# Kernel optimization log

Measured on AMD Instinct MI355X. Metric: run time of the kernel, lower is better.

Reference implementation:

```python
import jax, jax.numpy as jnp
import numpy as np

N_NODES = 50000
N_EDGES = 1_600_000
IN_DIM = 256
HIDDEN = 256
OUT_DIM = 48
K = 10
ALPHA = 0.5


def _ppr_temp(K, alpha):
    # PPR init from GPR_prop: temp[k] = alpha*(1-alpha)^k, temp[K] = (1-alpha)^K
    t = alpha * (1 - alpha) ** np.arange(K + 1, dtype=np.float32)
    t[-1] = (1 - alpha) ** K
    return jnp.asarray(t, dtype=jnp.float32)


def setup_inputs() -> dict:
    key = jax.random.key(0)
    ks = jax.random.split(key, 7)
    x = jax.random.normal(ks[0], (N_NODES, IN_DIM), dtype=jnp.float32)
    edge_index = jax.random.randint(ks[1], (2, N_EDGES), 0, N_NODES, dtype=jnp.int64)
    # Linear layers (torch Linear: y = x @ W.T + b); store as [in, out]
    lim1 = 1.0 / np.sqrt(IN_DIM)
    W1 = jax.random.uniform(ks[2], (IN_DIM, HIDDEN), jnp.float32, -lim1, lim1)
    b1 = jax.random.uniform(ks[3], (HIDDEN,), jnp.float32, -lim1, lim1)
    lim2 = 1.0 / np.sqrt(HIDDEN)
    W2 = jax.random.uniform(ks[4], (HIDDEN, OUT_DIM), jnp.float32, -lim2, lim2)
    b2 = jax.random.uniform(ks[5], (OUT_DIM,), jnp.float32, -lim2, lim2)
    temp = _ppr_temp(K, ALPHA)
    return {"x": x, "edge_index": edge_index, "W1": W1, "b1": b1,
            "W2": W2, "b2": b2, "temp": temp}


def reference(x, edge_index, W1, b1, W2, b2, temp):
    N = x.shape[0]
    # MLP head (dropout in eval mode -> identity)
    h = jax.nn.relu(x @ W1 + b1)
    h = h @ W2 + b2  # [N, OUT_DIM]

    # GCN normalization with self-loops: norm_e = deg^-1/2[src] * deg^-1/2[dst]
    loops = jnp.arange(N, dtype=edge_index.dtype)
    src = jnp.concatenate([edge_index[0], loops])
    dst = jnp.concatenate([edge_index[1], loops])
    deg = jnp.zeros((N,), dtype=h.dtype).at[dst].add(1.0)
    dinv = jax.lax.rsqrt(jnp.maximum(deg, 1e-12))
    norm = (dinv[src] * dinv[dst])[:, None]  # [E+N, 1]

    # K-hop propagation with learned gamma mixing
    def step(carry, gamma):
        hk, hidden = carry
        msg = norm * hk[src]                              # gather + scale
        hk = jax.ops.segment_sum(msg, dst, num_segments=N)  # scatter-add
        return (hk, hidden + gamma * hk), None

    (_, hidden), _ = jax.lax.scan(step, (h, temp[0] * h), temp[1:])
    return jax.nn.log_softmax(hidden, axis=1)
```

## Files before the change

kernel.cpp:

```cpp
#include <hip/hip_runtime.h>
#include <hip/hip_fp16.h>
#include <math.h>

#define BSH    9
#define BNODES 512
#define NBMAX  128
#define CAP2   24576
#define ECHUNK 6144

typedef short bf16x8 __attribute__((ext_vector_type(8)));
typedef float f32x4 __attribute__((ext_vector_type(4)));

__device__ __forceinline__ unsigned f2b(float f) {
    union { float f; unsigned u; } x; x.f = f;
    return (x.u + 0x7fffu + ((x.u >> 16) & 1u)) >> 16;
}


__global__ __launch_bounds__(256) void k_zero(int* __restrict__ p, int n) {
    int i = blockIdx.x * 256 + threadIdx.x;
    if (i < n) p[i] = 0;
}


__global__ __launch_bounds__(256) void k_castx(const float4* __restrict__ x, uint4* __restrict__ xb, int n8) {
    int i = blockIdx.x * 256 + threadIdx.x;
    if (i >= n8) return;
    float4 f0 = x[2 * i], f1 = x[2 * i + 1];
    uint4 o;
    o.x = f2b(f0.x) | (f2b(f0.y) << 16);
    o.y = f2b(f0.z) | (f2b(f0.w) << 16);
    o.z = f2b(f1.x) | (f2b(f1.y) << 16);
    o.w = f2b(f1.z) | (f2b(f1.w) << 16);
    xb[i] = o;
}

__global__ __launch_bounds__(256) void k_castw(const float* __restrict__ W1, const float* __restrict__ W2,
                                               unsigned short* __restrict__ w1t, unsigned short* __restrict__ w2t) {
    int i = blockIdx.x * 256 + threadIdx.x;
    if (i < 65536) {
        int n = i >> 8, k = i & 255;
        w1t[i] = (unsigned short)f2b(W1[k * 256 + n]);
    } else if (i < 65536 + 12288) {
        int j = i - 65536;
        int n = j >> 8, k = j & 255;
        w2t[j] = (unsigned short)f2b(W2[k * 48 + n]);
    }
}


__global__ __launch_bounds__(256) void k_bin(const int* __restrict__ src, const int* __restrict__ dst,
                                             int* __restrict__ bktcnt, unsigned* __restrict__ stage,
                                             int E, int NB) {
    __shared__ unsigned ecache[ECHUNK];
    __shared__ int lcnt[NBMAX], lbase[NBMAX], lcur[NBMAX];
    const int t = threadIdx.x;
    for (int i = t; i < NBMAX; i += 256) { lcnt[i] = 0; lcur[i] = 0; }
    const int e0 = blockIdx.x * ECHUNK;
    const int m = min(ECHUNK, E - e0);
    __syncthreads();
    for (int i = t; i < m; i += 256) {
        int s = src[e0 + i], d = dst[e0 + i];
        ecache[i] = ((unsigned)d << 16) | (unsigned)s;
        atomicAdd(&lcnt[d >> BSH], 1);
    }
    __syncthreads();
    if (t < NB) lbase[t] = lcnt[t] ? atomicAdd(&bktcnt[t], lcnt[t]) : 0;
    __syncthreads();
    for (int i = t; i < m; i += 256) {
        unsigned p = ecache[i];
        int b = (int)(p >> (16 + BSH));
        int pos = lbase[b] + atomicAdd(&lcur[b], 1);
        if (pos < CAP2) stage[(size_t)b * CAP2 + pos] = p;
    }
}


__global__ __launch_bounds__(512) void k_cnt(const unsigned* __restrict__ stage,
                                             const int* __restrict__ bktcnt,
                                             int* __restrict__ cnt,
                                             float* __restrict__ dinv, float* __restrict__ dinv2,
                                             float* __restrict__ sdeg, int N) {
    __shared__ int dcnt[BNODES];
    const int b = blockIdx.x, t = threadIdx.x;
    dcnt[t] = 0;
    __syncthreads();
    const int m = min(bktcnt[b], CAP2);
    const unsigned* st = stage + (size_t)b * CAP2;
    for (int i = t; i < m; i += 512)
        atomicAdd(&dcnt[(st[i] >> 16) & (BNODES - 1)], 1);
    __syncthreads();
    int node = b * BNODES + t;
    if (node <= N) {
        int c = dcnt[t];
        cnt[node] = c;
        float d = (float)c + 1.0f;
        float r = rsqrtf(d);
        dinv[node] = r;
        dinv2[node] = r * r;
        sdeg[node] = d * r;
    }
}


__global__ __launch_bounds__(256) void k_scan1(const int* __restrict__ cnt, int* __restrict__ rowptr,
                                               int* __restrict__ blk, int NT) {
    __shared__ int s[256];
    int t = threadIdx.x, i = blockIdx.x * 256 + t;
    int v = (i < NT) ? ((cnt[i] + 31) & ~31) : 0;
    s[t] = v; __syncthreads();
#pragma unroll
    for (int off = 1; off < 256; off <<= 1) {
        int x = (t >= off) ? s[t - off] : 0; __syncthreads();
        s[t] += x; __syncthreads();
    }
    if (i < NT) rowptr[i] = s[t] - v;
    if (t == 255) blk[blockIdx.x] = s[255];
}

__global__ __launch_bounds__(256) void k_scan2(int* __restrict__ blk, int nb) {
    __shared__ int s[256];
    int t = threadIdx.x;
    int v = (t < nb) ? blk[t] : 0;
    s[t] = v; __syncthreads();
#pragma unroll
    for (int off = 1; off < 256; off <<= 1) {
        int x = (t >= off) ? s[t - off] : 0; __syncthreads();
        s[t] += x; __syncthreads();
    }
    if (t < nb) blk[t] = s[t] - v;
}

__global__ __launch_bounds__(256) void k_scan3(int* __restrict__ rowptr, const int* __restrict__ blk, int NT) {
    int i = blockIdx.x * 256 + threadIdx.x;
    if (i < NT) rowptr[i] += blk[blockIdx.x];
}


__global__ __launch_bounds__(512) void k_place(const unsigned* __restrict__ stage,
                                               const int* __restrict__ bktcnt,
                                               const int* __restrict__ rowptr,
                                               unsigned short* __restrict__ csr, int N) {
    __shared__ int lcur[BNODES];
    const int b = blockIdx.x, t = threadIdx.x;
    const int node = b * BNODES + t;
    lcur[t] = (node < N) ? rowptr[node] : 0;
    __syncthreads();
    const int m = min(bktcnt[b], CAP2);
    const unsigned* st = stage + (size_t)b * CAP2;
    for (int i = t; i < m; i += 512) {
        unsigned p = st[i];
        int dl = (int)((p >> 16) & (BNODES - 1));
        int pos = atomicAdd(&lcur[dl], 1);
        csr[pos] = (unsigned short)(p & 0xffffu);
    }
    __syncthreads();
    if (node < N) {
        int e1 = rowptr[node + 1];
        for (int i = lcur[t]; i < e1; ++i) csr[i] = (unsigned short)N;
    }
}


__global__ __launch_bounds__(256) void k_mgemm1(const unsigned short* __restrict__ xb,
                                                const unsigned short* __restrict__ w1t,
                                                const float* __restrict__ bias,
                                                unsigned short* __restrict__ h1b, int M) {
    __shared__ unsigned short sbuf[128 * 136];
    unsigned short* As = sbuf;
    unsigned short* Bs = sbuf + 128 * 40;
    const int t = threadIdx.x;
    const int bm = blockIdx.x * 128;
    const int bn = blockIdx.y * 128;
    const int w = t >> 6, lane = t & 63;
    const int q = lane >> 4, l16 = lane & 15;

    f32x4 acc[2][8] = {};
    const int ar0 = t >> 2;
    const int kc  = t & 3;
    const int swz_st = ((kc ^ (ar0 & 3)) * 8);
    int gr0 = bm + ar0;       if (gr0 >= M) gr0 = M - 1;
    int gr1 = bm + ar0 + 64;  if (gr1 >= M) gr1 = M - 1;
    const int swz_rd = (q ^ (l16 & 3)) * 8;

    for (int k0 = 0; k0 < 256; k0 += 32) {
        uint4 a0 = *(const uint4*)&xb[(size_t)gr0 * 256 + k0 + kc * 8];
        uint4 a1 = *(const uint4*)&xb[(size_t)gr1 * 256 + k0 + kc * 8];
        uint4 b0 = *(const uint4*)&w1t[(size_t)(bn + ar0) * 256 + k0 + kc * 8];
        uint4 b1 = *(const uint4*)&w1t[(size_t)(bn + ar0 + 64) * 256 + k0 + kc * 8];
        __syncthreads();
        *(uint4*)&As[ar0 * 40 + swz_st] = a0;
        *(uint4*)&As[(ar0 + 64) * 40 + swz_st] = a1;
        *(uint4*)&Bs[ar0 * 40 + swz_st] = b0;
        *(uint4*)&Bs[(ar0 + 64) * 40 + swz_st] = b1;
        __syncthreads();
        bf16x8 af0 = *(bf16x8*)&As[(w * 32 + l16) * 40 + swz_rd];
        bf16x8 af1 = *(bf16x8*)&As[(w * 32 + 16 + l16) * 40 + swz_rd];
#pragma unroll
        for (int j = 0; j < 8; ++j) {
            bf16x8 bf = *(bf16x8*)&Bs[(j * 16 + l16) * 40 + swz_rd];
            acc[0][j] = __builtin_amdgcn_mfma_f32_16x16x32_bf16(af0, bf, acc[0][j], 0, 0, 0);
            acc[1][j] = __builtin_amdgcn_mfma_f32_16x16x32_bf16(af1, bf, acc[1][j], 0, 0, 0);
        }
    }
    __syncthreads();
#pragma unroll
    for (int j = 0; j < 8; ++j) {
        int col = j * 16 + l16;
        float bb = bias[bn + col];
#pragma unroll
        for (int i = 0; i < 2; ++i) {
#pragma unroll
            for (int r = 0; r < 4; ++r) {
                float v = fmaxf(acc[i][j][r] + bb, 0.f);
                sbuf[(w * 32 + i * 16 + q * 4 + r) * 136 + col] = (unsigned short)f2b(v);
            }
        }
    }
    __syncthreads();
    const int row = t >> 1;
    const int ch = (t & 1) * 64;
    if (bm + row < M) {
#pragma unroll
        for (int i = 0; i < 8; ++i) {
            uint4 v = *(uint4*)&sbuf[row * 136 + ch + i * 8];
            *(uint4*)&h1b[(size_t)(bm + row) * 256 + bn + ch + i * 8] = v;
        }
    }
}


__global__ __launch_bounds__(256) void k_mgemm2(const unsigned short* __restrict__ h1b,
                                                const unsigned short* __restrict__ w2t,
                                                const float* __restrict__ bias,
                                                const float* __restrict__ dinv,
                                                __half* __restrict__ u0, int M) {
    __shared__ unsigned short As[128 * 40];
    __shared__ unsigned short Bs[48 * 40];
    const int t = threadIdx.x;
    const int bm = blockIdx.x * 128;
    const int w = t >> 6, lane = t & 63;
    const int q = lane >> 4, l16 = lane & 15;

    f32x4 acc[2][3] = {};
    const int ar0 = t >> 2;
    const int kc  = t & 3;
    const int swz_st = ((kc ^ (ar0 & 3)) * 8);
    int gr0 = bm + ar0;      if (gr0 >= M) gr0 = M - 1;
    int gr1 = bm + ar0 + 64; if (gr1 >= M) gr1 = M - 1;
    const int swz_rd = (q ^ (l16 & 3)) * 8;

    for (int k0 = 0; k0 < 256; k0 += 32) {
        uint4 a0 = *(const uint4*)&h1b[(size_t)gr0 * 256 + k0 + kc * 8];
        uint4 a1 = *(const uint4*)&h1b[(size_t)gr1 * 256 + k0 + kc * 8];
        uint4 bv;
        if (t < 192) bv = *(const uint4*)&w2t[(size_t)ar0 * 256 + k0 + kc * 8];
        __syncthreads();
        *(uint4*)&As[ar0 * 40 + swz_st] = a0;
        *(uint4*)&As[(ar0 + 64) * 40 + swz_st] = a1;
        if (t < 192) *(uint4*)&Bs[ar0 * 40 + swz_st] = bv;
        __syncthreads();
        bf16x8 af0 = *(bf16x8*)&As[(w * 32 + l16) * 40 + swz_rd];
        bf16x8 af1 = *(bf16x8*)&As[(w * 32 + 16 + l16) * 40 + swz_rd];
#pragma unroll
        for (int j = 0; j < 3; ++j) {
            bf16x8 bf = *(bf16x8*)&Bs[(j * 16 + l16) * 40 + swz_rd];
            acc[0][j] = __builtin_amdgcn_mfma_f32_16x16x32_bf16(af0, bf, acc[0][j], 0, 0, 0);
            acc[1][j] = __builtin_amdgcn_mfma_f32_16x16x32_bf16(af1, bf, acc[1][j], 0, 0, 0);
        }
    }
#pragma unroll
    for (int j = 0; j < 3; ++j) {
        int col = j * 16 + l16;
        float bb = bias[col];
#pragma unroll
        for (int i = 0; i < 2; ++i) {
#pragma unroll
            for (int r = 0; r < 4; ++r) {
                int row = bm + w * 32 + i * 16 + q * 4 + r;
                if (row < M) {
                    float v = (acc[i][j][r] + bb) * dinv[row];
                    u0[(size_t)row * 48 + col] = __float2half(v);
                }
            }
        }
    }
}


__global__ __launch_bounds__(256) void k_hop(const __half* __restrict__ u, __half* __restrict__ unxt,
                                             const int* __restrict__ rowptr,
                                             const unsigned short* __restrict__ csr,
                                             const float* __restrict__ dinv2, int NT) {
    int n = blockIdx.x * 4 + (threadIdx.x >> 6);
    if (n >= NT) return;
    const int lane = threadIdx.x & 63;
    const int j = lane & 7;
    const int cc = lane >> 3;
    const bool act = cc < 6;
    const int ccs = act ? cc : 0;

    float acc[8] = {0.f, 0.f, 0.f, 0.f, 0.f, 0.f, 0.f, 0.f};
    int e0 = rowptr[n], e1 = rowptr[n + 1];
    for (int e = e0; e < e1; e += 32) {
        int sa = (int)csr[e + j];
        int sb = (int)csr[e + 8 + j];
        int sc = (int)csr[e + 16 + j];
        int sd = (int)csr[e + 24 + j];
        union { uint4 u4; __half2 h2[4]; } ga, gb, gc, gd;
        ga.u4 = *(const uint4*)(u + (size_t)sa * 48 + ccs * 8);
        gb.u4 = *(const uint4*)(u + (size_t)sb * 48 + ccs * 8);
        gc.u4 = *(const uint4*)(u + (size_t)sc * 48 + ccs * 8);
        gd.u4 = *(const uint4*)(u + (size_t)sd * 48 + ccs * 8);
#pragma unroll
        for (int i = 0; i < 4; ++i) {
            float2 fa = __half22float2(ga.h2[i]);
            float2 fb = __half22float2(gb.h2[i]);
            float2 fc = __half22float2(gc.h2[i]);
            float2 fd = __half22float2(gd.h2[i]);
            acc[2 * i]     += (fa.x + fb.x) + (fc.x + fd.x);
            acc[2 * i + 1] += (fa.y + fb.y) + (fc.y + fd.y);
        }
    }
#pragma unroll
    for (int off = 1; off < 8; off <<= 1) {
#pragma unroll
        for (int i = 0; i < 8; ++i) acc[i] += __shfl_xor(acc[i], off);
    }
    if (act && j == 0) {
        union { uint4 u4; __half2 h2[4]; } sv, ov;
        sv.u4 = *(const uint4*)(u + (size_t)n * 48 + cc * 8);
        float w2 = dinv2[n];
#pragma unroll
        for (int i = 0; i < 4; ++i) {
            float2 sf = __half22float2(sv.h2[i]);
            float2 r;
            r.x = (acc[2 * i]     + sf.x) * w2;
            r.y = (acc[2 * i + 1] + sf.y) * w2;
            ov.h2[i] = __float22half2_rn(r);
        }
        *(uint4*)(unxt + (size_t)n * 48 + cc * 8) = ov.u4;
    }
}


__global__ __launch_bounds__(256) void k_final(const __half* __restrict__ u0, const __half* __restrict__ u1,
                                               size_t S, const float* __restrict__ sdeg,
                                               const float* __restrict__ temp,
                                               float* __restrict__ out, int N) {
    int w = (blockIdx.x * 256 + threadIdx.x) >> 6;
    int lane = threadIdx.x & 63;
    if (w >= N) return;
    size_t base = (size_t)w * 48 + lane;
    float val = 0.f, m = -INFINITY;
    if (lane < 48) {
        float acc = temp[0] * __half2float(u0[base]);
        const __half* uk = u1;
#pragma unroll
        for (int k = 1; k <= 10; ++k) {
            acc += temp[k] * __half2float(uk[base]);
            uk += S;
        }
        val = acc * sdeg[w];
        m = val;
    }
#pragma unroll
    for (int off = 32; off; off >>= 1) m = fmaxf(m, __shfl_xor(m, off));
    float ex = (lane < 48) ? __expf(val - m) : 0.f;
    float s = ex;
#pragma unroll
    for (int off = 32; off; off >>= 1) s += __shfl_xor(s, off);
    if (lane < 48) out[(size_t)w * 48 + lane] = val - m - __logf(s);
}


extern "C" void kernel_launch(void* const* d_in, const int* in_sizes, int n_in,
                              void* d_out, int out_size, void* d_ws, size_t ws_size,
                              hipStream_t stream) {
    const float* x    = (const float*)d_in[0];
    const int*   ei   = (const int*)d_in[1];
    const float* W1   = (const float*)d_in[2];
    const float* b1   = (const float*)d_in[3];
    const float* W2   = (const float*)d_in[4];
    const float* b2   = (const float*)d_in[5];
    const float* temp = (const float*)d_in[6];
    float* out = (float*)d_out;

    const int N = in_sizes[0] / 256;
    const int E = in_sizes[1] / 2;
    const int* src = ei;
    const int* dst = ei + E;

    const int NT  = N + 1;
    const int NT2 = N + 2;
    const int NB  = (NT + BNODES - 1) >> BSH;

    char* w8 = (char*)d_ws;
    size_t NP = (size_t)((NT2 + 63) & ~63);
    int*   cnt     = (int*)w8;
    int*   bktcnt  = cnt + NP;
    int*   rowptr  = bktcnt + 128;
    int*   blk     = rowptr + NP;
    float* dinv    = (float*)(blk + 256);
    float* dinv2   = dinv + NP;
    float* sdeg    = dinv2 + NP;
    unsigned short* csr = (unsigned short*)(sdeg + NP);
    size_t csr_i   = (((size_t)E + 32 * NT) / 2 + 32 + 63) & ~(size_t)63;
    unsigned short* w1t = (unsigned short*)((int*)(sdeg + NP) + csr_i);
    unsigned short* w2t = w1t + 65536;
    unsigned short* xb  = w2t + 12288 + 64;
    size_t S       = ((size_t)NT * 48 + 127) & ~(size_t)127;
    __half* u0     = (__half*)(xb + (size_t)N * 256);
    unsigned short* h1b = (unsigned short*)(u0 + S);
    unsigned* stage = (unsigned*)h1b;
    __half* u1     = (__half*)(h1b + (size_t)N * 256);

    const int nbS = (NT2 + 255) / 256;

    k_zero  <<<(int)((NP + 128 + 255) / 256), 256, 0, stream>>>(cnt, (int)(NP + 128));
    k_bin   <<<(E + ECHUNK - 1) / ECHUNK, 256, 0, stream>>>(src, dst, bktcnt, stage, E, NB);
    k_cnt   <<<NB, 512, 0, stream>>>(stage, bktcnt, cnt, dinv, dinv2, sdeg, N);
    k_scan1 <<<nbS, 256, 0, stream>>>(cnt, rowptr, blk, NT2);
    k_scan2 <<<1, 256, 0, stream>>>(blk, nbS);
    k_scan3 <<<nbS, 256, 0, stream>>>(rowptr, blk, NT2);
    k_place <<<NB, 512, 0, stream>>>(stage, bktcnt, rowptr, csr, N);

    k_castx <<<(N * 256 / 8 + 255) / 256, 256, 0, stream>>>((const float4*)x, (uint4*)xb, N * 256 / 8);
    k_castw <<<(65536 + 12288 + 255) / 256, 256, 0, stream>>>(W1, W2, w1t, w2t);

    dim3 g1((N + 127) / 128, 2);
    k_mgemm1<<<g1, 256, 0, stream>>>(xb, w1t, b1, h1b, N);
    k_mgemm2<<<(N + 127) / 128, 256, 0, stream>>>(h1b, w2t, b2, dinv, u0, N);
    k_zero  <<<1, 64, 0, stream>>>((int*)(u0 + (size_t)N * 48), 24);

    const int hopBlocks = (NT + 3) / 4;
    for (int k = 0; k < 10; ++k) {
        const __half* cur = (k == 0) ? u0 : (u1 + (size_t)(k - 1) * S);
        __half* nxt = u1 + (size_t)k * S;
        k_hop<<<hopBlocks, 256, 0, stream>>>(cur, nxt, rowptr, csr, dinv2, NT);
    }

    k_final<<<(N + 3) / 4, 256, 0, stream>>>(u0, u1, S, sdeg, temp, out, N);
}
```

Baseline: 506.9 us.

## Fuse x bf16 cast into GEMM1, shrink CSR row padding, add hop tail loop

```diff
diff --git a/kernel.cpp b/kernel.cpp
--- a/kernel.cpp
+++ b/kernel.cpp
@@ -20,19 +20,6 @@
 __global__ __launch_bounds__(256) void k_zero(int* __restrict__ p, int n) {
     int i = blockIdx.x * 256 + threadIdx.x;
     if (i < n) p[i] = 0;
-}
-
-
-__global__ __launch_bounds__(256) void k_castx(const float4* __restrict__ x, uint4* __restrict__ xb, int n8) {
-    int i = blockIdx.x * 256 + threadIdx.x;
-    if (i >= n8) return;
-    float4 f0 = x[2 * i], f1 = x[2 * i + 1];
-    uint4 o;
-    o.x = f2b(f0.x) | (f2b(f0.y) << 16);
-    o.y = f2b(f0.z) | (f2b(f0.w) << 16);
-    o.z = f2b(f1.x) | (f2b(f1.y) << 16);
-    o.w = f2b(f1.z) | (f2b(f1.w) << 16);
-    xb[i] = o;
 }
 
 __global__ __launch_bounds__(256) void k_castw(const float* __restrict__ W1, const float* __restrict__ W2,
@@ -107,7 +94,7 @@
                                                int* __restrict__ blk, int NT) {
     __shared__ int s[256];
     int t = threadIdx.x, i = blockIdx.x * 256 + t;
-    int v = (i < NT) ? ((cnt[i] + 31) & ~31) : 0;
+    int v = (i < NT) ? ((cnt[i] + 7) & ~7) : 0;
     s[t] = v; __syncthreads();
 #pragma unroll
     for (int off = 1; off < 256; off <<= 1) {
@@ -162,7 +149,7 @@
 }
 
 
-__global__ __launch_bounds__(256) void k_mgemm1(const unsigned short* __restrict__ xb,
+__global__ __launch_bounds__(256) void k_mgemm1(const float* __restrict__ x,
                                                 const unsigned short* __restrict__ w1t,
                                                 const float* __restrict__ bias,
                                                 unsigned short* __restrict__ h1b, int M) {
@@ -184,10 +171,21 @@
     const int swz_rd = (q ^ (l16 & 3)) * 8;
 
     for (int k0 = 0; k0 < 256; k0 += 32) {
-        uint4 a0 = *(const uint4*)&xb[(size_t)gr0 * 256 + k0 + kc * 8];
-        uint4 a1 = *(const uint4*)&xb[(size_t)gr1 * 256 + k0 + kc * 8];
+        float4 f0 = *(const float4*)&x[(size_t)gr0 * 256 + k0 + kc * 8];
+        float4 f1 = *(const float4*)&x[(size_t)gr0 * 256 + k0 + kc * 8 + 4];
+        float4 f2 = *(const float4*)&x[(size_t)gr1 * 256 + k0 + kc * 8];
+        float4 f3 = *(const float4*)&x[(size_t)gr1 * 256 + k0 + kc * 8 + 4];
         uint4 b0 = *(const uint4*)&w1t[(size_t)(bn + ar0) * 256 + k0 + kc * 8];
         uint4 b1 = *(const uint4*)&w1t[(size_t)(bn + ar0 + 64) * 256 + k0 + kc * 8];
+        uint4 a0, a1;
+        a0.x = f2b(f0.x) | (f2b(f0.y) << 16);
+        a0.y = f2b(f0.z) | (f2b(f0.w) << 16);
+        a0.z = f2b(f1.x) | (f2b(f1.y) << 16);
+        a0.w = f2b(f1.z) | (f2b(f1.w) << 16);
+        a1.x = f2b(f2.x) | (f2b(f2.y) << 16);
+        a1.y = f2b(f2.z) | (f2b(f2.w) << 16);
+        a1.z = f2b(f3.x) | (f2b(f3.y) << 16);
+        a1.w = f2b(f3.z) | (f2b(f3.w) << 16);
         __syncthreads();
         *(uint4*)&As[ar0 * 40 + swz_st] = a0;
         *(uint4*)&As[(ar0 + 64) * 40 + swz_st] = a1;
@@ -302,7 +300,8 @@
 
     float acc[8] = {0.f, 0.f, 0.f, 0.f, 0.f, 0.f, 0.f, 0.f};
     int e0 = rowptr[n], e1 = rowptr[n + 1];
-    for (int e = e0; e < e1; e += 32) {
+    int e = e0;
+    for (; e + 32 <= e1; e += 32) {
         int sa = (int)csr[e + j];
         int sb = (int)csr[e + 8 + j];
         int sc = (int)csr[e + 16 + j];
@@ -314,12 +313,23 @@
         gd.u4 = *(const uint4*)(u + (size_t)sd * 48 + ccs * 8);
 #pragma unroll
         for (int i = 0; i < 4; ++i) {
+            __half2 p = __hadd2(ga.h2[i], gb.h2[i]);
+            __half2 qq = __hadd2(gc.h2[i], gd.h2[i]);
+            float2 fp = __half22float2(p);
+            float2 fq = __half22float2(qq);
+            acc[2 * i]     += fp.x + fq.x;
+            acc[2 * i + 1] += fp.y + fq.y;
+        }
+    }
+    for (; e < e1; e += 8) {
+        int sa = (int)csr[e + j];
+        union { uint4 u4; __half2 h2[4]; } ga;
+        ga.u4 = *(const uint4*)(u + (size_t)sa * 48 + ccs * 8);
+#pragma unroll
+        for (int i = 0; i < 4; ++i) {
             float2 fa = __half22float2(ga.h2[i]);
-            float2 fb = __half22float2(gb.h2[i]);
-            float2 fc = __half22float2(gc.h2[i]);
-            float2 fd = __half22float2(gd.h2[i]);
-            acc[2 * i]     += (fa.x + fb.x) + (fc.x + fd.x);
-            acc[2 * i + 1] += (fa.y + fb.y) + (fc.y + fd.y);
+            acc[2 * i]     += fa.x;
+            acc[2 * i + 1] += fa.y;
         }
     }
 #pragma unroll
@@ -408,9 +418,8 @@
     size_t csr_i   = (((size_t)E + 32 * NT) / 2 + 32 + 63) & ~(size_t)63;
     unsigned short* w1t = (unsigned short*)((int*)(sdeg + NP) + csr_i);
     unsigned short* w2t = w1t + 65536;
-    unsigned short* xb  = w2t + 12288 + 64;
     size_t S       = ((size_t)NT * 48 + 127) & ~(size_t)127;
-    __half* u0     = (__half*)(xb + (size_t)N * 256);
+    __half* u0     = (__half*)(w2t + 12288 + 64);
     unsigned short* h1b = (unsigned short*)(u0 + S);
     unsigned* stage = (unsigned*)h1b;
     __half* u1     = (__half*)(h1b + (size_t)N * 256);
@@ -425,11 +434,10 @@
     k_scan3 <<<nbS, 256, 0, stream>>>(rowptr, blk, NT2);
     k_place <<<NB, 512, 0, stream>>>(stage, bktcnt, rowptr, csr, N);
 
-    k_castx <<<(N * 256 / 8 + 255) / 256, 256, 0, stream>>>((const float4*)x, (uint4*)xb, N * 256 / 8);
     k_castw <<<(65536 + 12288 + 255) / 256, 256, 0, stream>>>(W1, W2, w1t, w2t);
 
     dim3 g1((N + 127) / 128, 2);
-    k_mgemm1<<<g1, 256, 0, stream>>>(xb, w1t, b1, h1b, N);
+    k_mgemm1<<<g1, 256, 0, stream>>>(x, w1t, b1, h1b, N);
     k_mgemm2<<<(N + 127) / 128, 256, 0, stream>>>(h1b, w2t, b2, dinv, u0, N);
     k_zero  <<<1, 64, 0, stream>>>((int*)(u0 + (size_t)N * 48), 24);
 
```

Measured after the change: 489.2 us. -3.5%, faster.

## Pad propagation rows to 64 halves and split hop into two column-half kernels

Applied to the files above, without the earlier changes.

```diff
diff --git a/kernel.cpp b/kernel.cpp
--- a/kernel.cpp
+++ b/kernel.cpp
@@ -280,7 +280,7 @@
                 int row = bm + w * 32 + i * 16 + q * 4 + r;
                 if (row < M) {
                     float v = (acc[i][j][r] + bb) * dinv[row];
-                    u0[(size_t)row * 48 + col] = __float2half(v);
+                    u0[(size_t)row * 64 + col] = __float2half(v);
                 }
             }
         }
@@ -288,48 +288,36 @@
 }
 
 
-__global__ __launch_bounds__(256) void k_hop(const __half* __restrict__ u, __half* __restrict__ unxt,
-                                             const int* __restrict__ rowptr,
-                                             const unsigned short* __restrict__ csr,
-                                             const float* __restrict__ dinv2, int NT) {
+__global__ __launch_bounds__(256) void k_hopA(const __half* __restrict__ u, __half* __restrict__ unxt,
+                                              const int* __restrict__ rowptr,
+                                              const unsigned short* __restrict__ csr,
+                                              const float* __restrict__ dinv2, int NT) {
     int n = blockIdx.x * 4 + (threadIdx.x >> 6);
     if (n >= NT) return;
     const int lane = threadIdx.x & 63;
-    const int j = lane & 7;
-    const int cc = lane >> 3;
-    const bool act = cc < 6;
-    const int ccs = act ? cc : 0;
-
+    const int cc = lane & 3;
+    const int e  = lane >> 2;
     float acc[8] = {0.f, 0.f, 0.f, 0.f, 0.f, 0.f, 0.f, 0.f};
-    int e0 = rowptr[n], e1 = rowptr[n + 1];
-    for (int e = e0; e < e1; e += 32) {
-        int sa = (int)csr[e + j];
-        int sb = (int)csr[e + 8 + j];
-        int sc = (int)csr[e + 16 + j];
-        int sd = (int)csr[e + 24 + j];
-        union { uint4 u4; __half2 h2[4]; } ga, gb, gc, gd;
-        ga.u4 = *(const uint4*)(u + (size_t)sa * 48 + ccs * 8);
-        gb.u4 = *(const uint4*)(u + (size_t)sb * 48 + ccs * 8);
-        gc.u4 = *(const uint4*)(u + (size_t)sc * 48 + ccs * 8);
-        gd.u4 = *(const uint4*)(u + (size_t)sd * 48 + ccs * 8);
+    const int e0 = rowptr[n], e1 = rowptr[n + 1];
+    for (int eb = e0; eb < e1; eb += 16) {
+        int s = (int)csr[eb + e];
+        union { uint4 u4; __half2 h2[4]; } g;
+        g.u4 = *(const uint4*)(u + (size_t)s * 64 + cc * 8);
 #pragma unroll
         for (int i = 0; i < 4; ++i) {
-            float2 fa = __half22float2(ga.h2[i]);
-            float2 fb = __half22float2(gb.h2[i]);
-            float2 fc = __half22float2(gc.h2[i]);
-            float2 fd = __half22float2(gd.h2[i]);
-            acc[2 * i]     += (fa.x + fb.x) + (fc.x + fd.x);
-            acc[2 * i + 1] += (fa.y + fb.y) + (fc.y + fd.y);
-        }
-    }
-#pragma unroll
-    for (int off = 1; off < 8; off <<= 1) {
+            float2 f = __half22float2(g.h2[i]);
+            acc[2 * i]     += f.x;
+            acc[2 * i + 1] += f.y;
+        }
+    }
+#pragma unroll
+    for (int off = 4; off < 64; off <<= 1) {
 #pragma unroll
         for (int i = 0; i < 8; ++i) acc[i] += __shfl_xor(acc[i], off);
     }
-    if (act && j == 0) {
+    if (e == 0) {
         union { uint4 u4; __half2 h2[4]; } sv, ov;
-        sv.u4 = *(const uint4*)(u + (size_t)n * 48 + cc * 8);
+        sv.u4 = *(const uint4*)(u + (size_t)n * 64 + cc * 8);
         float w2 = dinv2[n];
 #pragma unroll
         for (int i = 0; i < 4; ++i) {
@@ -339,7 +327,50 @@
             r.y = (acc[2 * i + 1] + sf.y) * w2;
             ov.h2[i] = __float22half2_rn(r);
         }
-        *(uint4*)(unxt + (size_t)n * 48 + cc * 8) = ov.u4;
+        *(uint4*)(unxt + (size_t)n * 64 + cc * 8) = ov.u4;
+    }
+}
+
+__global__ __launch_bounds__(256) void k_hopB(const __half* __restrict__ u, __half* __restrict__ unxt,
+                                              const int* __restrict__ rowptr,
+                                              const unsigned short* __restrict__ csr,
+                                              const float* __restrict__ dinv2, int NT) {
+    int n = blockIdx.x * 4 + (threadIdx.x >> 6);
+    if (n >= NT) return;
+    const int lane = threadIdx.x & 63;
+    const int cc = lane & 1;
+    const int e  = lane >> 1;
+    float acc[8] = {0.f, 0.f, 0.f, 0.f, 0.f, 0.f, 0.f, 0.f};
+    const int e0 = rowptr[n], e1 = rowptr[n + 1];
+    for (int eb = e0; eb < e1; eb += 32) {
+        int s = (int)csr[eb + e];
+        union { uint4 u4; __half2 h2[4]; } g;
+        g.u4 = *(const uint4*)(u + (size_t)s * 64 + 32 + cc * 8);
+#pragma unroll
+        for (int i = 0; i < 4; ++i) {
+            float2 f = __half22float2(g.h2[i]);
+            acc[2 * i]     += f.x;
+            acc[2 * i + 1] += f.y;
+        }
+    }
+#pragma unroll
+    for (int off = 2; off < 64; off <<= 1) {
+#pragma unroll
+        for (int i = 0; i < 8; ++i) acc[i] += __shfl_xor(acc[i], off);
+    }
+    if (e == 0) {
+        union { uint4 u4; __half2 h2[4]; } sv, ov;
+        sv.u4 = *(const uint4*)(u + (size_t)n * 64 + 32 + cc * 8);
+        float w2 = dinv2[n];
+#pragma unroll
+        for (int i = 0; i < 4; ++i) {
+            float2 sf = __half22float2(sv.h2[i]);
+            float2 r;
+            r.x = (acc[2 * i]     + sf.x) * w2;
+            r.y = (acc[2 * i + 1] + sf.y) * w2;
+            ov.h2[i] = __float22half2_rn(r);
+        }
+        *(uint4*)(unxt + (size_t)n * 64 + 32 + cc * 8) = ov.u4;
     }
 }
 
@@ -351,7 +382,7 @@
     int w = (blockIdx.x * 256 + threadIdx.x) >> 6;
     int lane = threadIdx.x & 63;
     if (w >= N) return;
-    size_t base = (size_t)w * 48 + lane;
+    size_t base = (size_t)w * 64 + lane;
     float val = 0.f, m = -INFINITY;
     if (lane < 48) {
         float acc = temp[0] * __half2float(u0[base]);
@@ -409,7 +440,7 @@
     unsigned short* w1t = (unsigned short*)((int*)(sdeg + NP) + csr_i);
     unsigned short* w2t = w1t + 65536;
     unsigned short* xb  = w2t + 12288 + 64;
-    size_t S       = ((size_t)NT * 48 + 127) & ~(size_t)127;
+    size_t S       = ((size_t)NT * 64 + 127) & ~(size_t)127;
     __half* u0     = (__half*)(xb + (size_t)N * 256);
     unsigned short* h1b = (unsigned short*)(u0 + S);
     unsigned* stage = (unsigned*)h1b;
@@ -431,13 +462,14 @@
     dim3 g1((N + 127) / 128, 2);
     k_mgemm1<<<g1, 256, 0, stream>>>(xb, w1t, b1, h1b, N);
     k_mgemm2<<<(N + 127) / 128, 256, 0, stream>>>(h1b, w2t, b2, dinv, u0, N);
-    k_zero  <<<1, 64, 0, stream>>>((int*)(u0 + (size_t)N * 48), 24);
+    k_zero  <<<1, 64, 0, stream>>>((int*)(u0 + (size_t)N * 64), 24);
 
     const int hopBlocks = (NT + 3) / 4;
     for (int k = 0; k < 10; ++k) {
         const __half* cur = (k == 0) ? u0 : (u1 + (size_t)(k - 1) * S);
         __half* nxt = u1 + (size_t)k * S;
-        k_hop<<<hopBlocks, 256, 0, stream>>>(cur, nxt, rowptr, csr, dinv2, NT);
+        k_hopA<<<hopBlocks, 256, 0, stream>>>(cur, nxt, rowptr, csr, dinv2, NT);
+        k_hopB<<<hopBlocks, 256, 0, stream>>>(cur, nxt, rowptr, csr, dinv2, NT);
     }
 
     k_final<<<(N + 3) / 4, 256, 0, stream>>>(u0, u1, S, sdeg, temp, out, N);
```

After: 743.4 us. 1.47x slower.

## Pad feature rows to 64 halves and shrink CSR row padding to 8

Applied to the files above, without the earlier changes.

```diff
diff --git a/kernel.cpp b/kernel.cpp
--- a/kernel.cpp
+++ b/kernel.cpp
@@ -107,7 +107,7 @@
                                                int* __restrict__ blk, int NT) {
     __shared__ int s[256];
     int t = threadIdx.x, i = blockIdx.x * 256 + t;
-    int v = (i < NT) ? ((cnt[i] + 31) & ~31) : 0;
+    int v = (i < NT) ? ((cnt[i] + 7) & ~7) : 0;
     s[t] = v; __syncthreads();
 #pragma unroll
     for (int off = 1; off < 256; off <<= 1) {
@@ -280,7 +280,7 @@
                 int row = bm + w * 32 + i * 16 + q * 4 + r;
                 if (row < M) {
                     float v = (acc[i][j][r] + bb) * dinv[row];
-                    u0[(size_t)row * 48 + col] = __float2half(v);
+                    u0[(size_t)row * 64 + col] = __float2half(v);
                 }
             }
         }
@@ -295,41 +295,51 @@
     int n = blockIdx.x * 4 + (threadIdx.x >> 6);
     if (n >= NT) return;
     const int lane = threadIdx.x & 63;
-    const int j = lane & 7;
-    const int cc = lane >> 3;
-    const bool act = cc < 6;
-    const int ccs = act ? cc : 0;
+    const int c = lane & 7;
+    const int j = lane >> 3;
 
     float acc[8] = {0.f, 0.f, 0.f, 0.f, 0.f, 0.f, 0.f, 0.f};
-    int e0 = rowptr[n], e1 = rowptr[n + 1];
-    for (int e = e0; e < e1; e += 32) {
+    const int e0 = rowptr[n], e1 = rowptr[n + 1];
+    int e = e0;
+    for (; e + 32 <= e1; e += 32) {
         int sa = (int)csr[e + j];
         int sb = (int)csr[e + 8 + j];
         int sc = (int)csr[e + 16 + j];
         int sd = (int)csr[e + 24 + j];
         union { uint4 u4; __half2 h2[4]; } ga, gb, gc, gd;
-        ga.u4 = *(const uint4*)(u + (size_t)sa * 48 + ccs * 8);
-        gb.u4 = *(const uint4*)(u + (size_t)sb * 48 + ccs * 8);
-        gc.u4 = *(const uint4*)(u + (size_t)sc * 48 + ccs * 8);
-        gd.u4 = *(const uint4*)(u + (size_t)sd * 48 + ccs * 8);
+        ga.u4 = *(const uint4*)(u + (size_t)sa * 64 + c * 8);
+        gb.u4 = *(const uint4*)(u + (size_t)sb * 64 + c * 8);
+        gc.u4 = *(const uint4*)(u + (size_t)sc * 64 + c * 8);
+        gd.u4 = *(const uint4*)(u + (size_t)sd * 64 + c * 8);
+#pragma unroll
+        for (int i = 0; i < 4; ++i) {
+            __half2 p = __hadd2(ga.h2[i], gb.h2[i]);
+            __half2 qq = __hadd2(gc.h2[i], gd.h2[i]);
+            float2 fp = __half22float2(p);
+            float2 fq = __half22float2(qq);
+            acc[2 * i]     += fp.x + fq.x;
+            acc[2 * i + 1] += fp.y + fq.y;
+        }
+    }
+    for (; e < e1; e += 8) {
+        int sa = (int)csr[e + j];
+        union { uint4 u4; __half2 h2[4]; } ga;
+        ga.u4 = *(const uint4*)(u + (size_t)sa * 64 + c * 8);
 #pragma unroll
         for (int i = 0; i < 4; ++i) {
             float2 fa = __half22float2(ga.h2[i]);
-            float2 fb = __half22float2(gb.h2[i]);
-            float2 fc = __half22float2(gc.h2[i]);
-            float2 fd = __half22float2(gd.h2[i]);
-            acc[2 * i]     += (fa.x + fb.x) + (fc.x + fd.x);
-            acc[2 * i + 1] += (fa.y + fb.y) + (fc.y + fd.y);
-        }
-    }
-#pragma unroll
-    for (int off = 1; off < 8; off <<= 1) {
+            acc[2 * i]     += fa.x;
+            acc[2 * i + 1] += fa.y;
+        }
+    }
+#pragma unroll
+    for (int off = 8; off < 64; off <<= 1) {
 #pragma unroll
         for (int i = 0; i < 8; ++i) acc[i] += __shfl_xor(acc[i], off);
     }
-    if (act && j == 0) {
+    if (j == 0 && c < 6) {
         union { uint4 u4; __half2 h2[4]; } sv, ov;
-        sv.u4 = *(const uint4*)(u + (size_t)n * 48 + cc * 8);
+        sv.u4 = *(const uint4*)(u + (size_t)n * 64 + c * 8);
         float w2 = dinv2[n];
 #pragma unroll
         for (int i = 0; i < 4; ++i) {
@@ -339,7 +349,7 @@
             r.y = (acc[2 * i + 1] + sf.y) * w2;
             ov.h2[i] = __float22half2_rn(r);
         }
-        *(uint4*)(unxt + (size_t)n * 48 + cc * 8) = ov.u4;
+        *(uint4*)(unxt + (size_t)n * 64 + c * 8) = ov.u4;
     }
 }
 
@@ -351,7 +361,7 @@
     int w = (blockIdx.x * 256 + threadIdx.x) >> 6;
     int lane = threadIdx.x & 63;
     if (w >= N) return;
-    size_t base = (size_t)w * 48 + lane;
+    size_t base = (size_t)w * 64 + lane;
     float val = 0.f, m = -INFINITY;
     if (lane < 48) {
         float acc = temp[0] * __half2float(u0[base]);
@@ -409,7 +419,7 @@
     unsigned short* w1t = (unsigned short*)((int*)(sdeg + NP) + csr_i);
     unsigned short* w2t = w1t + 65536;
     unsigned short* xb  = w2t + 12288 + 64;
-    size_t S       = ((size_t)NT * 48 + 127) & ~(size_t)127;
+    size_t S       = ((size_t)NT * 64 + 127) & ~(size_t)127;
     __half* u0     = (__half*)(xb + (size_t)N * 256);
     unsigned short* h1b = (unsigned short*)(u0 + S);
     unsigned* stage = (unsigned*)h1b;
@@ -431,7 +441,7 @@
     dim3 g1((N + 127) / 128, 2);
     k_mgemm1<<<g1, 256, 0, stream>>>(xb, w1t, b1, h1b, N);
     k_mgemm2<<<(N + 127) / 128, 256, 0, stream>>>(h1b, w2t, b2, dinv, u0, N);
-    k_zero  <<<1, 64, 0, stream>>>((int*)(u0 + (size_t)N * 48), 24);
+    k_zero  <<<1, 64, 0, stream>>>((int*)(u0 + (size_t)N * 64), 24);
 
     const int hopBlocks = (NT + 3) / 4;
     for (int k = 0; k < 10; ++k) {
```

New measurement: 461.7 us, median of 2. 8.9% less time.
